# Kernel optimization log

Measured on AMD Instinct MI355X. Metric: run time of the kernel, lower is better.

Reference implementation:

```python
import jax, jax.numpy as jnp
import numpy as np

NUM_HEADS = 16
HEAD_DIM = 128
HIDDEN = NUM_HEADS * HEAD_DIM  # 2048
ROPE_BASE = 10000.0


def _rope_tables(seq_len, dtype=jnp.float32):
    inv_freq = 1.0 / (ROPE_BASE ** (jnp.arange(0, HEAD_DIM, 2, dtype=jnp.float32) / HEAD_DIM))
    freqs = jnp.arange(seq_len, dtype=jnp.float32)[:, None] * inv_freq[None, :]  # [S, hd/2]
    return jnp.cos(freqs).astype(dtype), jnp.sin(freqs).astype(dtype)


def _apply_rope(x, cos, sin):
    # x: [B, S, H, hd]; interleaved even/odd rotation
    B, S, H, D = x.shape
    xr = x.reshape(B, S, H, D // 2, 2)
    x_even, x_odd = xr[..., 0], xr[..., 1]
    c = cos[None, :, None, :]
    s = sin[None, :, None, :]
    rot_even = x_even * c - x_odd * s
    rot_odd = x_even * s + x_odd * c
    return jnp.stack([rot_even, rot_odd], axis=-1).reshape(B, S, H, D)


def setup_inputs() -> dict:
    key = jax.random.key(0)
    k1, k2, k3, k4, k5 = jax.random.split(key, 5)
    B, S = 2, 2048
    hidden_states = jax.random.normal(k1, (B, S, HIDDEN), dtype=jnp.float32)
    attention_mask = jnp.zeros((B, 1, 1, S), dtype=jnp.float32)
    scale = 1.0 / np.sqrt(HIDDEN)
    Wqkv = jax.random.normal(k2, (3 * HIDDEN, HIDDEN), dtype=jnp.float32) * scale
    bqkv = jnp.zeros((3 * HIDDEN,), dtype=jnp.float32)
    Wout = jax.random.normal(k3, (HIDDEN, HIDDEN), dtype=jnp.float32) * scale
    bout = jnp.zeros((HIDDEN,), dtype=jnp.float32)
    return {"hidden_states": hidden_states, "attention_mask": attention_mask,
            "Wqkv": Wqkv, "bqkv": bqkv, "Wout": Wout, "bout": bout}


def reference(hidden_states, attention_mask, Wqkv, bqkv, Wout, bout):
    B, S, _ = hidden_states.shape
    scale = 1.0 / np.sqrt(HEAD_DIM)
    qkv = hidden_states @ Wqkv.T + bqkv                      # [B, S, 3*HIDDEN]
    qkv = qkv.reshape(B, S, 3, NUM_HEADS, HEAD_DIM)
    q, k, v = qkv[:, :, 0], qkv[:, :, 1], qkv[:, :, 2]       # [B, S, H, hd]
    cos, sin = _rope_tables(S, hidden_states.dtype)
    q = _apply_rope(q, cos, sin)
    k = _apply_rope(k, cos, sin)
    scores = jnp.einsum('bqhd,bkhd->bhqk', q, k) * scale     # [B, H, S, S]
    scores = scores + attention_mask
    probs = jax.nn.softmax(scores, axis=-1)
    ctx = jnp.einsum('bhqk,bkhd->bqhd', probs, v)            # [B, S, H, hd]
    ctx = ctx.reshape(B, S, HIDDEN)
    return ctx @ Wout.T + bout
```

## Files before the change

kernel.cpp:

```cpp
#include <hip/hip_runtime.h>
#include <math.h>

#define HID    2048
#define NH     16
#define HD     128
#define SEQ    2048
#define NBATCH 2
#define NT     (SEQ / 64)

typedef __attribute__((ext_vector_type(8))) short bf16x8;
typedef __attribute__((ext_vector_type(4))) float f32x4;

__device__ __forceinline__ short f2bf(float f) {
    union { float f; unsigned u; } x; x.f = f;
    unsigned r = x.u + 0x7fffu + ((x.u >> 16) & 1u);
    return (short)(r >> 16);
}
__device__ __forceinline__ float bf2f(short s) {
    union { unsigned u; float f; } y;
    y.u = ((unsigned)(unsigned short)s) << 16;
    return y.f;
}

__device__ __forceinline__ void gl_lds16(const short* g, short* l) {
    __builtin_amdgcn_global_load_lds(
        (const __attribute__((address_space(1))) unsigned int*)g,
        (__attribute__((address_space(3))) unsigned int*)l, 16, 0, 0);
}

#define ROPE_N  (SEQ * 64)
#define HS_N4   (NBATCH * SEQ * HID / 4)
#define WQKV_N4 (3 * HID * HID / 4)
#define WOUT_N4 (HID * HID / 4)

__global__ __launch_bounds__(256) void prep_kernel(
    const float* __restrict__ hs, const float* __restrict__ Wqkv,
    const float* __restrict__ Wout,
    float2* __restrict__ cst, short* __restrict__ Ahs,
    short* __restrict__ Wqkvh, short* __restrict__ Wouth) {
    const long total = (long)ROPE_N + HS_N4 + WQKV_N4 + WOUT_N4;
    for (long idx = (long)blockIdx.x * 256 + threadIdx.x; idx < total;
         idx += (long)gridDim.x * 256) {
        if (idx < ROPE_N) {
            int s = (int)(idx >> 6);
            int i = (int)(idx & 63);
            double inv = pow(10000.0, -(double)i / 64.0);
            float freq = (float)s * (float)inv;
            float2 cs = make_float2(cosf(freq), sinf(freq));
            cst[s * HD + 2 * i]     = cs;
            cst[s * HD + 2 * i + 1] = cs;
        } else if (idx < (long)ROPE_N + HS_N4) {
            long i = idx - ROPE_N;
            float4 v = ((const float4*)hs)[i];
            short4 h;
            h.x = f2bf(v.x); h.y = f2bf(v.y); h.z = f2bf(v.z); h.w = f2bf(v.w);
            *(short4*)(Ahs + 4 * i) = h;
        } else if (idx < (long)ROPE_N + HS_N4 + WQKV_N4) {
            long i = idx - ROPE_N - HS_N4;
            float4 v = ((const float4*)Wqkv)[i];
            short4 h;
            h.x = f2bf(v.x); h.y = f2bf(v.y); h.z = f2bf(v.z); h.w = f2bf(v.w);
            *(short4*)(Wqkvh + 4 * i) = h;
        } else {
            long i = idx - ROPE_N - HS_N4 - WQKV_N4;
            float4 v = ((const float4*)Wout)[i];
            short4 h;
            h.x = f2bf(v.x); h.y = f2bf(v.y); h.z = f2bf(v.z); h.w = f2bf(v.w);
            *(short4*)(Wouth + 4 * i) = h;
        }
    }
}

#define LDSA 0
#define LDSB 4096

__global__ __launch_bounds__(256, 3) void gemm_out_kernel(
    const short* __restrict__ Ah, const short* __restrict__ Bh,
    const float* __restrict__ bias, float* __restrict__ C) {
    __shared__ short lds[8192];

    const int t     = threadIdx.x;
    const int w     = t >> 6;
    const int lane  = t & 63;
    const int mfrag = lane & 15;
    const int quad  = lane >> 4;
    const int wm    = (w >> 1) * 64;
    const int wn    = (w & 1) * 64;
    const int m0    = blockIdx.y * 128;
    const int n0    = blockIdx.x * 128;

    const int srow   = lane >> 2;
    const int schunk = (((lane & 3) ^ ((lane >> 3) & 3))) * 8;
    const short* gA0 = Ah + (size_t)(m0 + w * 16 + srow) * HID + schunk;
    const short* gA1 = Ah + (size_t)(m0 + 64 + w * 16 + srow) * HID + schunk;
    const short* gB0 = Bh + (size_t)(n0 + w * 16 + srow) * HID + schunk;
    const short* gB1 = Bh + (size_t)(n0 + 64 + w * 16 + srow) * HID + schunk;
    short* lA0 = &lds[LDSA + (w * 16) * 32];
    short* lA1 = &lds[LDSA + (64 + w * 16) * 32];
    short* lB0 = &lds[LDSB + (w * 16) * 32];
    short* lB1 = &lds[LDSB + (64 + w * 16) * 32];

    const int chA = 8 * (quad ^ ((mfrag >> 1) & 3));

    f32x4 acc[4][4];
#pragma unroll
    for (int i = 0; i < 4; ++i)
#pragma unroll
        for (int j = 0; j < 4; ++j) acc[i][j] = (f32x4){0.f, 0.f, 0.f, 0.f};

    for (int kt = 0; kt < HID; kt += 32) {
        __syncthreads();
        gl_lds16(gA0 + kt, lA0);
        gl_lds16(gA1 + kt, lA1);
        gl_lds16(gB0 + kt, lB0);
        gl_lds16(gB1 + kt, lB1);
        __syncthreads();

        bf16x8 ah[4], bh[4];
#pragma unroll
        for (int mt = 0; mt < 4; ++mt)
            ah[mt] = *(const bf16x8*)&lds[LDSA + (wm + mt * 16 + mfrag) * 32 + chA];
#pragma unroll
        for (int nt = 0; nt < 4; ++nt)
            bh[nt] = *(const bf16x8*)&lds[LDSB + (wn + nt * 16 + mfrag) * 32 + chA];

#pragma unroll
        for (int mt = 0; mt < 4; ++mt)
#pragma unroll
            for (int nt = 0; nt < 4; ++nt)
                acc[mt][nt] = __builtin_amdgcn_mfma_f32_16x16x32_bf16(
                    ah[mt], bh[nt], acc[mt][nt], 0, 0, 0);
    }

    float bcol[4];
#pragma unroll
    for (int nt = 0; nt < 4; ++nt) bcol[nt] = bias[n0 + wn + nt * 16 + mfrag];

#pragma unroll
    for (int mt = 0; mt < 4; ++mt)
#pragma unroll
        for (int r = 0; r < 4; ++r) {
            int mm = m0 + wm + mt * 16 + 4 * quad + r;
#pragma unroll
            for (int nt = 0; nt < 4; ++nt)
                C[(size_t)mm * HID + n0 + wn + nt * 16 + mfrag] =
                    acc[mt][nt][r] + bcol[nt];
        }
}

#define PR1 __builtin_amdgcn_s_setprio(1)
#define PR0 __builtin_amdgcn_s_setprio(0)
#define BARX __builtin_amdgcn_s_barrier()
#define LGKM0 asm volatile("s_waitcnt lgkmcnt(0)" ::: "memory")
#define VMC(n) asm volatile("s_waitcnt vmcnt(" #n ")" ::: "memory")

#define STAGE_AH(bf, ke, hh) { _Pragma("unroll") for (int c = 0; c < 2; ++c) \
    gl_lds16(Ag + (size_t)(((hh) * 2 + c) * 64) * HID + (ke), \
             &lds[(bf) * 32768 + sdst + ((hh) * 2 + c) * 4096]); }
#define STAGE_BH(bf, ke, hh) { _Pragma("unroll") for (int c = 0; c < 2; ++c) \
    gl_lds16(Bg + (size_t)(((hh) * 2 + c) * 64) * HID + (ke), \
             &lds[(bf) * 32768 + 16384 + sdst + ((hh) * 2 + c) * 4096]); }

#define LOADA(bf, mh) { _Pragma("unroll") for (int x = 0; x < 4; ++x) { \
    aF[x][0] = *(const bf16x8*)&lds[(bf) * 32768 + aoff + ((mh) * 4 + x) * 1024 + fc0]; \
    aF[x][1] = *(const bf16x8*)&lds[(bf) * 32768 + aoff + ((mh) * 4 + x) * 1024 + fc1]; } }
#define LOADB(bf, nh, dstF) { _Pragma("unroll") for (int x = 0; x < 2; ++x) { \
    dstF[x][0] = *(const bf16x8*)&lds[(bf) * 32768 + 16384 + boff + ((nh) * 2 + x) * 1024 + fc0]; \
    dstF[x][1] = *(const bf16x8*)&lds[(bf) * 32768 + 16384 + boff + ((nh) * 2 + x) * 1024 + fc1]; } }
#define QUADM(mh, nh, bF) { _Pragma("unroll") for (int x = 0; x < 4; ++x) \
    _Pragma("unroll") for (int y = 0; y < 2; ++y) { \
    acc[(mh) * 4 + x][(nh) * 2 + y] = __builtin_amdgcn_mfma_f32_16x16x32_bf16( \
        aF[x][0], bF[y][0], acc[(mh) * 4 + x][(nh) * 2 + y], 0, 0, 0); \
    acc[(mh) * 4 + x][(nh) * 2 + y] = __builtin_amdgcn_mfma_f32_16x16x32_bf16( \
        aF[x][1], bF[y][1], acc[(mh) * 4 + x][(nh) * 2 + y], 0, 0, 0); } }

__global__ __launch_bounds__(512, 2) void gemm256_qkv_kernel(
    const short* __restrict__ Ah, const short* __restrict__ Bh,
    const float* __restrict__ bias,
    short* __restrict__ qb, short* __restrict__ kbf, short* __restrict__ vTt,
    const float2* __restrict__ cst) {
    __shared__ __align__(16) short lds[65536];

    const int t    = threadIdx.x;
    const int w    = t >> 6;
    const int lane = t & 63;
    const int m    = lane & 15;
    const int quad = lane >> 4;
    const int wm   = w >> 2;
    const int wn   = w & 3;

    const int swz = (blockIdx.x & 7) * 48 + (blockIdx.x >> 3);
    const int bx  = swz / 16;
    const int by  = swz % 16;
    const int m0  = by * 256;
    const int n0  = bx * 256;

    const int srl = lane >> 3;
    const int sch = ((lane & 7) ^ (srl & 7)) * 8;
    const short* Ag = Ah + (size_t)(m0 + w * 8 + srl) * HID + sch;
    const short* Bg = Bh + (size_t)(n0 + w * 8 + srl) * HID + sch;
    const int sdst  = w * 512;

    const int key  = m & 7;
    const int fc0  = (quad ^ key) * 8;
    const int fc1  = ((4 + quad) ^ key) * 8;
    const int aoff = (wm * 128 + m) * 64;
    const int boff = (wn * 64 + m) * 64;

    f32x4 acc[8][4];
#pragma unroll
    for (int i = 0; i < 8; ++i)
#pragma unroll
        for (int j = 0; j < 4; ++j) acc[i][j] = (f32x4){0.f, 0.f, 0.f, 0.f};

    bf16x8 aF[4][2], b0F[2][2], b1F[2][2];

    STAGE_AH(0, 0, 0); STAGE_AH(0, 0, 1);
    STAGE_BH(0, 0, 0); STAGE_BH(0, 0, 1);
    STAGE_BH(1, 64, 0); STAGE_BH(1, 64, 1);
    VMC(4); BARX;

    const int NIT = HID / 128;
#pragma unroll 1
    for (int i = 0; i < NIT; ++i) {
        const int k1   = i * 128 + 64;
        const int k2   = (i + 1) * 128;
        const int k3   = k2 + 64;
        const bool more = (i + 1 < NIT);
        LOADA(0, 0); LOADB(0, 0, b0F);
        STAGE_AH(1, k1, 0);
        BARX; LGKM0; PR1; QUADM(0, 0, b0F); PR0; BARX;
        LOADB(0, 1, b1F);
        STAGE_AH(1, k1, 1);
        BARX; LGKM0; PR1; QUADM(0, 1, b1F); PR0; BARX;
        LOADA(0, 1);
        if (more) STAGE_BH(0, k2, 0);
        BARX; LGKM0; PR1; QUADM(1, 1, b1F); PR0; BARX;
        if (more) { STAGE_BH(0, k2, 1); VMC(4); } else { VMC(0); }
        BARX; PR1; QUADM(1, 0, b0F); PR0; BARX;
        LOADA(1, 0); LOADB(1, 0, b0F);
        if (more) STAGE_AH(0, k2, 0);
        BARX; LGKM0; PR1; QUADM(0, 0, b0F); PR0; BARX;
        LOADB(1, 1, b1F);
        if (more) STAGE_AH(0, k2, 1);
        BARX; LGKM0; PR1; QUADM(0, 1, b1F); PR0; BARX;
        LOADA(1, 1);
        if (more) STAGE_BH(1, k3, 0);
        BARX; LGKM0; PR1; QUADM(1, 1, b1F); PR0; BARX;
        if (more) { STAGE_BH(1, k3, 1); VMC(4); }
        BARX; PR1; QUADM(1, 0, b0F); PR0; BARX;
    }

    const int which = n0 >> 11;
    const int bidx  = m0 >> 11;
    const int cb    = (n0 & 2047) + wn * 64;
    const int h     = cb >> 7;
    const int d0    = cb & 127;

    float bcol[4];
#pragma unroll
    for (int nt = 0; nt < 4; ++nt) bcol[nt] = bias[n0 + wn * 64 + nt * 16 + m];

    if (which < 2) {
        short* dst = (which == 0) ? qb : kbf;
        const float post = (which == 0) ? 0.08838834764831845f : 1.0f;
#pragma unroll
        for (int mt = 0; mt < 8; ++mt)
#pragma unroll
            for (int r = 0; r < 4; ++r) {
                int sl = (m0 & 2047) + wm * 128 + mt * 16 + 4 * quad + r;
                const float2* csr = cst + (size_t)sl * HD;
                size_t rowb = ((size_t)(bidx * NH + h) * SEQ + sl) * HD;
#pragma unroll
                for (int nt = 0; nt < 4; ++nt) {
                    float x  = acc[mt][nt][r] + bcol[nt];
                    float px = __shfl_xor(x, 1, 64);
                    int   d  = d0 + nt * 16 + m;
                    float2 cs = csr[d];
                    float rot = (m & 1) ? fmaf(px, cs.y, x * cs.x)
                                        : (x * cs.x - px * cs.y);
                    dst[rowb + d] = f2bf(rot * post);
                }
            }
    } else {
        short* tw = &lds[w * 8192];
#pragma unroll
        for (int mt = 0; mt < 8; ++mt)
#pragma unroll
            for (int nt = 0; nt < 4; ++nt)
#pragma unroll
                for (int r = 0; r < 4; ++r) {
                    int s_l = mt * 16 + 4 * quad + r;
                    int d_l = nt * 16 + m;
                    tw[d_l * 128 + (((s_l >> 3) ^ m) << 3) + (s_l & 7)] =
                        f2bf(acc[mt][nt][r] + bcol[nt]);
                }
        const size_t vbase = (size_t)(bidx * NH + h) * HD * SEQ;
        const int sbase = (m0 & 2047) + wm * 128;
#pragma unroll
        for (int it = 0; it < 16; ++it) {
            int d_l = it * 4 + quad;
            bf16x8 row = *(const bf16x8*)&tw[d_l * 128 + ((m ^ (d_l & 15)) << 3)];
            *(bf16x8*)(vTt + vbase + (size_t)(d0 + d_l) * SEQ + sbase + m * 8) = row;
        }
    }
}

#define AK0 0
#define AK1 8192
#define AV0 16384
#define AV1 24576
#define AP  32768

__global__ __launch_bounds__(512, 4) void attn_mfma_kernel(
    const short* __restrict__ qb, const short* __restrict__ kbf,
    const short* __restrict__ vTt, const float* __restrict__ mask,
    short* __restrict__ ctxb) {
    __shared__ __align__(16) short lds[40960];

    const int t    = threadIdx.x;
    const int w    = t >> 6;
    const int lane = t & 63;
    const int m    = lane & 15;
    const int quad = lane >> 4;

    const int id  = blockIdx.x;
    const int j   = id >> 3;
    const int bh  = (id & 7) * 4 + (j >> 4);
    const int q0  = (j & 15) * 128;
    const int b   = bh >> 4;
    const int h   = bh & 15;

    const size_t base = (size_t)bh * SEQ * HD;
    const short* kp = kbf + base;
    const short* vp = vTt + base;
    const float* mrow = mask + (size_t)b * SEQ;

    size_t kOff[2], vOff[2];
    int kDst[2], vDst[2];
#pragma unroll
    for (int u = 0; u < 2; ++u) {
        int rk = w * 8 + u * 4 + (lane >> 4);
        int ck = (lane & 15) ^ (rk & 7);
        kOff[u] = (size_t)rk * HD + ck * 8;
        kDst[u] = (w * 8 + u * 4) * 128;
        int rv = w * 16 + u * 8 + (lane >> 3);
        int cv = (lane & 7) ^ (rv & 7);
        vOff[u] = (size_t)rv * SEQ + cv * 8;
        vDst[u] = (w * 16 + u * 8) * 64;
    }

    const int srow = q0 + w * 16 + m;
    bf16x8 qh[4];
    {
        const short* qhp = qb + base + (size_t)srow * HD;
#pragma unroll
        for (int c = 0; c < 4; ++c)
            qh[c] = *(const bf16x8*)(qhp + 32 * c + 8 * quad);
    }

    f32x4 O[8];
    float m_i[4], l_p[4];
#pragma unroll
    for (int c = 0; c < 8; ++c) O[c] = (f32x4){0.f, 0.f, 0.f, 0.f};
#pragma unroll
    for (int r = 0; r < 4; ++r) { m_i[r] = -INFINITY; l_p[r] = 0.f; }

    const int sw = m & 7;
    const int pb = AP + w * 1024;
    const int kcb = (m >> 3);
    const int ml  = m & 7;

#pragma unroll
    for (int u = 0; u < 2; ++u) {
        gl_lds16(kp + kOff[u], &lds[AK0 + kDst[u]]);
        gl_lds16(vp + vOff[u], &lds[AV0 + vDst[u]]);
    }

    for (int kt = 0; kt < NT; ++kt) {
        const int cur = kt & 1;
        const int k0  = kt * 64;

        __syncthreads();

        if (kt + 1 < NT) {
            const int nk0 = (kt + 1) * 64;
            const int nb  = cur ^ 1;
#pragma unroll
            for (int u = 0; u < 2; ++u) {
                gl_lds16(kp + (size_t)nk0 * HD + kOff[u],
                         &lds[(nb ? AK1 : AK0) + kDst[u]]);
                gl_lds16(vp + nk0 + vOff[u],
                         &lds[(nb ? AV1 : AV0) + vDst[u]]);
            }
        }

        const short* kb = &lds[cur ? AK1 : AK0];
        const short* vb = &lds[cur ? AV1 : AV0];

        float mk[4];
#pragma unroll
        for (int c2 = 0; c2 < 4; ++c2) mk[c2] = mrow[k0 + 16 * c2 + m];

        f32x4 S[4];
        __builtin_amdgcn_s_setprio(1);
#pragma unroll
        for (int c2 = 0; c2 < 4; ++c2) {
            f32x4 acc = (f32x4){0.f, 0.f, 0.f, 0.f};
#pragma unroll
            for (int c = 0; c < 4; ++c) {
                int pk = (4 * c + quad) ^ sw;
                bf16x8 kf = *(const bf16x8*)&kb[(16 * c2 + m) * 128 + pk * 8];
                acc = __builtin_amdgcn_mfma_f32_16x16x32_bf16(qh[c], kf, acc, 0, 0, 0);
            }
            S[c2] = acc;
        }
        __builtin_amdgcn_s_setprio(0);

        float rm4[4];
#pragma unroll
        for (int r = 0; r < 4; ++r) {
            float s0 = S[0][r] + mk[0];
            float s1 = S[1][r] + mk[1];
            float s2 = S[2][r] + mk[2];
            float s3 = S[3][r] + mk[3];
            S[0][r] = s0; S[1][r] = s1; S[2][r] = s2; S[3][r] = s3;
            float rm = fmaxf(fmaxf(s0, s1), fmaxf(s2, s3));
#pragma unroll
            for (int off = 1; off < 16; off <<= 1)
                rm = fmaxf(rm, __shfl_xor(rm, off, 64));
            rm4[r] = rm;
        }
        int needI = (rm4[0] > m_i[0] + 8.f) | (rm4[1] > m_i[1] + 8.f) |
                    (rm4[2] > m_i[2] + 8.f) | (rm4[3] > m_i[3] + 8.f);
        if (__any(needI)) {
#pragma unroll
            for (int r = 0; r < 4; ++r) {
                float mn = fmaxf(m_i[r], rm4[r]);
                float a  = __expf(m_i[r] - mn);
                m_i[r]   = mn;
                l_p[r]  *= a;
#pragma unroll
                for (int c = 0; c < 8; ++c) O[c][r] *= a;
            }
        }
        float p[4][4];
#pragma unroll
        for (int r = 0; r < 4; ++r) {
#pragma unroll
            for (int c2 = 0; c2 < 4; ++c2) p[c2][r] = __expf(S[c2][r] - m_i[r]);
            l_p[r] += (p[0][r] + p[1][r]) + (p[2][r] + p[3][r]);
        }

#pragma unroll
        for (int c2 = 0; c2 < 4; ++c2) {
#pragma unroll
            for (int jj = 0; jj < 2; ++jj) {
                unsigned pkw;
                asm("v_cvt_pk_bf16_f32 %0, %1, %2"
                    : "=v"(pkw) : "v"(p[c2][2 * jj]), "v"(p[c2][2 * jj + 1]));
                int ql = 4 * quad + 2 * jj;
                int qh2 = ql + 1;
                lds[pb + ql * 64 + (((2 * c2 + kcb) ^ (ql & 7)) << 3) + ml] =
                    (short)(pkw & 0xffffu);
                lds[pb + qh2 * 64 + (((2 * c2 + kcb) ^ (qh2 & 7)) << 3) + ml] =
                    (short)(pkw >> 16);
            }
        }

        __builtin_amdgcn_s_setprio(1);
#pragma unroll
        for (int cc = 0; cc < 2; ++cc) {
            int pv = (4 * cc + quad) ^ sw;
            bf16x8 pf = *(const bf16x8*)&lds[pb + m * 64 + (pv << 3)];
#pragma unroll
            for (int c = 0; c < 8; ++c) {
                bf16x8 vf = *(const bf16x8*)&vb[(16 * c + m) * 64 + pv * 8];
                O[c] = __builtin_amdgcn_mfma_f32_16x16x32_bf16(pf, vf, O[c], 0, 0, 0);
            }
        }
        __builtin_amdgcn_s_setprio(0);
    }

#pragma unroll
    for (int r = 0; r < 4; ++r) {
        float lv = l_p[r];
#pragma unroll
        for (int off = 1; off < 16; off <<= 1) lv += __shfl_xor(lv, off, 64);
        float inv = 1.0f / lv;
        int s = q0 + w * 16 + 4 * quad + r;
        size_t off2 = ((size_t)(b * SEQ + s)) * HID + h * HD;
#pragma unroll
        for (int c = 0; c < 8; ++c)
            ctxb[off2 + 16 * c + m] = f2bf(O[c][r] * inv);
    }
}

extern "C" void kernel_launch(void* const* d_in, const int* in_sizes, int n_in,
                              void* d_out, int out_size, void* d_ws, size_t ws_size,
                              hipStream_t stream) {
    const float* hs   = (const float*)d_in[0];
    const float* mask = (const float*)d_in[1];
    const float* Wqkv = (const float*)d_in[2];
    const float* bqkv = (const float*)d_in[3];
    const float* Wout = (const float*)d_in[4];
    const float* bout = (const float*)d_in[5];
    float* out = (float*)d_out;

    const size_t qkv_elems = (size_t)NBATCH * NH * SEQ * HD;
    char* p = (char*)d_ws;
    float2* cst  = (float2*)p; p += (size_t)SEQ * HD * 8;
    short* qbf   = (short*)p; p += qkv_elems * 2;
    short* kbf   = (short*)p; p += qkv_elems * 2;
    short* vTt   = (short*)p; p += qkv_elems * 2;
    short* Wqkvh = (short*)p; p += (size_t)3 * HID * HID * 2;
    short* Wouth = (short*)p; p += (size_t)HID * HID * 2;
    short* Ahs   = (short*)p; p += qkv_elems * 2;
    short* ctxb  = Ahs;

    prep_kernel<<<2048, 256, 0, stream>>>(hs, Wqkv, Wout, cst, Ahs, Wqkvh, Wouth);

    gemm256_qkv_kernel<<<384, 512, 0, stream>>>(
        Ahs, Wqkvh, bqkv, qbf, kbf, vTt, cst);

    attn_mfma_kernel<<<512, 512, 0, stream>>>(qbf, kbf, vTt, mask, ctxb);

    gemm_out_kernel<<<dim3(16, 32), 256, 0, stream>>>(ctxb, Wouth, bout, out);
}
```

Before: 415.9 us.

## Halve QKV GEMM LDS footprint with K=32 stages to double occupancy

The QKV projection GEMM now stages 32-wide K slices instead of 64-wide, halving shared memory from 128KB to 64KB, and launch bounds are raised from 2 to 4 blocks per CU. The pipeline is rebuilt around 64-K iterations with full vmcnt(0) waits, and the V-transpose epilogue is split into two halves serialized by __syncthreads so it fits the smaller LDS. This trades deeper prefetch and fewer barriers for more resident waves, with a risk of register spills under the tighter bound and more exposed memory latency.

```diff
diff --git a/kernel.cpp b/kernel.cpp
--- a/kernel.cpp
+++ b/kernel.cpp
@@ -154,32 +154,28 @@
 #define LGKM0 asm volatile("s_waitcnt lgkmcnt(0)" ::: "memory")
 #define VMC(n) asm volatile("s_waitcnt vmcnt(" #n ")" ::: "memory")
 
-#define STAGE_AH(bf, ke, hh) { _Pragma("unroll") for (int c = 0; c < 2; ++c) \
-    gl_lds16(Ag + (size_t)(((hh) * 2 + c) * 64) * HID + (ke), \
-             &lds[(bf) * 32768 + sdst + ((hh) * 2 + c) * 4096]); }
-#define STAGE_BH(bf, ke, hh) { _Pragma("unroll") for (int c = 0; c < 2; ++c) \
-    gl_lds16(Bg + (size_t)(((hh) * 2 + c) * 64) * HID + (ke), \
-             &lds[(bf) * 32768 + 16384 + sdst + ((hh) * 2 + c) * 4096]); }
-
-#define LOADA(bf, mh) { _Pragma("unroll") for (int x = 0; x < 4; ++x) { \
-    aF[x][0] = *(const bf16x8*)&lds[(bf) * 32768 + aoff + ((mh) * 4 + x) * 1024 + fc0]; \
-    aF[x][1] = *(const bf16x8*)&lds[(bf) * 32768 + aoff + ((mh) * 4 + x) * 1024 + fc1]; } }
-#define LOADB(bf, nh, dstF) { _Pragma("unroll") for (int x = 0; x < 2; ++x) { \
-    dstF[x][0] = *(const bf16x8*)&lds[(bf) * 32768 + 16384 + boff + ((nh) * 2 + x) * 1024 + fc0]; \
-    dstF[x][1] = *(const bf16x8*)&lds[(bf) * 32768 + 16384 + boff + ((nh) * 2 + x) * 1024 + fc1]; } }
+#define STAGE_A32(bf, ke, c) \
+    gl_lds16(Ag + (size_t)((c) * 128) * HID + (ke), \
+             &lds[(bf) * 16384 + sdst + (c) * 4096]);
+#define STAGE_B32(bf, ke, c) \
+    gl_lds16(Bg + (size_t)((c) * 128) * HID + (ke), \
+             &lds[(bf) * 16384 + 8192 + sdst + (c) * 4096]);
+
+#define LOADA(bf, mh) { _Pragma("unroll") for (int x = 0; x < 4; ++x) \
+    aF[x] = *(const bf16x8*)&lds[(bf) * 16384 + aoff + ((mh) * 4 + x) * 512 + fcA]; }
+#define LOADB(bf, nh, dstF) { _Pragma("unroll") for (int y = 0; y < 2; ++y) \
+    dstF[y] = *(const bf16x8*)&lds[(bf) * 16384 + 8192 + boff + ((nh) * 2 + y) * 512 + fcA]; }
 #define QUADM(mh, nh, bF) { _Pragma("unroll") for (int x = 0; x < 4; ++x) \
-    _Pragma("unroll") for (int y = 0; y < 2; ++y) { \
+    _Pragma("unroll") for (int y = 0; y < 2; ++y) \
     acc[(mh) * 4 + x][(nh) * 2 + y] = __builtin_amdgcn_mfma_f32_16x16x32_bf16( \
-        aF[x][0], bF[y][0], acc[(mh) * 4 + x][(nh) * 2 + y], 0, 0, 0); \
-    acc[(mh) * 4 + x][(nh) * 2 + y] = __builtin_amdgcn_mfma_f32_16x16x32_bf16( \
-        aF[x][1], bF[y][1], acc[(mh) * 4 + x][(nh) * 2 + y], 0, 0, 0); } }
-
-__global__ __launch_bounds__(512, 2) void gemm256_qkv_kernel(
+        aF[x], bF[y], acc[(mh) * 4 + x][(nh) * 2 + y], 0, 0, 0); }
+
+__global__ __launch_bounds__(512, 4) void gemm256_qkv_kernel(
     const short* __restrict__ Ah, const short* __restrict__ Bh,
     const float* __restrict__ bias,
     short* __restrict__ qb, short* __restrict__ kbf, short* __restrict__ vTt,
     const float2* __restrict__ cst) {
-    __shared__ __align__(16) short lds[65536];
+    __shared__ __align__(16) short lds[32768];
 
     const int t    = threadIdx.x;
     const int w    = t >> 6;
@@ -195,17 +191,15 @@
     const int m0  = by * 256;
     const int n0  = bx * 256;
 
-    const int srl = lane >> 3;
-    const int sch = ((lane & 7) ^ (srl & 7)) * 8;
-    const short* Ag = Ah + (size_t)(m0 + w * 8 + srl) * HID + sch;
-    const short* Bg = Bh + (size_t)(n0 + w * 8 + srl) * HID + sch;
+    const int srl = lane >> 2;
+    const int sch = ((lane & 3) ^ (srl & 3)) * 8;
+    const short* Ag = Ah + (size_t)(m0 + w * 16 + srl) * HID + sch;
+    const short* Bg = Bh + (size_t)(n0 + w * 16 + srl) * HID + sch;
     const int sdst  = w * 512;
 
-    const int key  = m & 7;
-    const int fc0  = (quad ^ key) * 8;
-    const int fc1  = ((4 + quad) ^ key) * 8;
-    const int aoff = (wm * 128 + m) * 64;
-    const int boff = (wn * 64 + m) * 64;
+    const int fcA  = (quad ^ (m & 3)) * 8;
+    const int aoff = (wm * 128 + m) * 32;
+    const int boff = (wn * 64 + m) * 32;
 
     f32x4 acc[8][4];
 #pragma unroll
@@ -213,41 +207,37 @@
 #pragma unroll
         for (int j = 0; j < 4; ++j) acc[i][j] = (f32x4){0.f, 0.f, 0.f, 0.f};
 
-    bf16x8 aF[4][2], b0F[2][2], b1F[2][2];
-
-    STAGE_AH(0, 0, 0); STAGE_AH(0, 0, 1);
-    STAGE_BH(0, 0, 0); STAGE_BH(0, 0, 1);
-    STAGE_BH(1, 64, 0); STAGE_BH(1, 64, 1);
-    VMC(4); BARX;
-
-    const int NIT = HID / 128;
+    bf16x8 aF[4], b0F[2], b1F[2];
+
+    STAGE_A32(0, 0, 0); STAGE_A32(0, 0, 1);
+    STAGE_B32(0, 0, 0); STAGE_B32(0, 0, 1);
+    VMC(0); BARX;
+
+    const int NIT = HID / 64;
 #pragma unroll 1
     for (int i = 0; i < NIT; ++i) {
-        const int k1   = i * 128 + 64;
-        const int k2   = (i + 1) * 128;
-        const int k3   = k2 + 64;
+        const int k1   = i * 64 + 32;
+        const int k2   = (i + 1) * 64;
         const bool more = (i + 1 < NIT);
         LOADA(0, 0); LOADB(0, 0, b0F);
-        STAGE_AH(1, k1, 0);
+        STAGE_A32(1, k1, 0); STAGE_A32(1, k1, 1);
         BARX; LGKM0; PR1; QUADM(0, 0, b0F); PR0; BARX;
         LOADB(0, 1, b1F);
-        STAGE_AH(1, k1, 1);
+        STAGE_B32(1, k1, 0); STAGE_B32(1, k1, 1);
         BARX; LGKM0; PR1; QUADM(0, 1, b1F); PR0; BARX;
         LOADA(0, 1);
-        if (more) STAGE_BH(0, k2, 0);
         BARX; LGKM0; PR1; QUADM(1, 1, b1F); PR0; BARX;
-        if (more) { STAGE_BH(0, k2, 1); VMC(4); } else { VMC(0); }
+        VMC(0);
         BARX; PR1; QUADM(1, 0, b0F); PR0; BARX;
         LOADA(1, 0); LOADB(1, 0, b0F);
-        if (more) STAGE_AH(0, k2, 0);
+        if (more) { STAGE_A32(0, k2, 0); STAGE_A32(0, k2, 1); }
         BARX; LGKM0; PR1; QUADM(0, 0, b0F); PR0; BARX;
         LOADB(1, 1, b1F);
-        if (more) STAGE_AH(0, k2, 1);
+        if (more) { STAGE_B32(0, k2, 0); STAGE_B32(0, k2, 1); }
         BARX; LGKM0; PR1; QUADM(0, 1, b1F); PR0; BARX;
         LOADA(1, 1);
-        if (more) STAGE_BH(1, k3, 0);
         BARX; LGKM0; PR1; QUADM(1, 1, b1F); PR0; BARX;
-        if (more) { STAGE_BH(1, k3, 1); VMC(4); }
+        VMC(0);
         BARX; PR1; QUADM(1, 0, b0F); PR0; BARX;
     }
 
@@ -283,25 +273,33 @@
                 }
             }
     } else {
-        short* tw = &lds[w * 8192];
-#pragma unroll
-        for (int mt = 0; mt < 8; ++mt)
-#pragma unroll
-            for (int nt = 0; nt < 4; ++nt)
-#pragma unroll
-                for (int r = 0; r < 4; ++r) {
-                    int s_l = mt * 16 + 4 * quad + r;
-                    int d_l = nt * 16 + m;
-                    tw[d_l * 128 + (((s_l >> 3) ^ m) << 3) + (s_l & 7)] =
-                        f2bf(acc[mt][nt][r] + bcol[nt]);
-                }
+        short* tw = &lds[(w & 3) * 8192];
         const size_t vbase = (size_t)(bidx * NH + h) * HD * SEQ;
         const int sbase = (m0 & 2047) + wm * 128;
 #pragma unroll
-        for (int it = 0; it < 16; ++it) {
-            int d_l = it * 4 + quad;
-            bf16x8 row = *(const bf16x8*)&tw[d_l * 128 + ((m ^ (d_l & 15)) << 3)];
-            *(bf16x8*)(vTt + vbase + (size_t)(d0 + d_l) * SEQ + sbase + m * 8) = row;
+        for (int half = 0; half < 2; ++half) {
+            if ((w >> 2) == half) {
+#pragma unroll
+                for (int mt = 0; mt < 8; ++mt)
+#pragma unroll
+                    for (int nt = 0; nt < 4; ++nt)
+#pragma unroll
+                        for (int r = 0; r < 4; ++r) {
+                            int s_l = mt * 16 + 4 * quad + r;
+                            int d_l = nt * 16 + m;
+                            tw[d_l * 128 + (((s_l >> 3) ^ m) << 3) + (s_l & 7)] =
+                                f2bf(acc[mt][nt][r] + bcol[nt]);
+                        }
+#pragma unroll
+                for (int it = 0; it < 16; ++it) {
+                    int d_l = it * 4 + quad;
+                    bf16x8 row = *(const bf16x8*)&tw[d_l * 128 +
+                                                    ((m ^ (d_l & 15)) << 3)];
+                    *(bf16x8*)(vTt + vbase + (size_t)(d0 + d_l) * SEQ +
+                               sbase + m * 8) = row;
+                }
+            }
+            __syncthreads();
         }
     }
 }
```

New measurement: 1.290 ms. 210% more time.
